# Optimization experiments

Hardware: AMD Instinct MI355X
Metric: run time of the kernel (lower is better)

Reference implementation:

```python
import jax, jax.numpy as jnp
import numpy as np

B, T_ENC, IN, H, TGT = 128, 128, 3, 512, 32

def setup_inputs() -> dict:
    key = jax.random.key(0)
    ks = jax.random.split(key, 16)
    s = 0.05
    return {
        "x": jax.random.normal(ks[0], (B, T_ENC, IN), jnp.float32),
        "y": jax.random.normal(ks[1], (B, TGT, 1), jnp.float32),
        # encoder: 2 layers x 2 directions (dim0 = [fwd, bwd])
        "enc_Wih0": jax.random.normal(ks[2], (2, H, IN), jnp.float32) * s,
        "enc_Whh0": jax.random.normal(ks[3], (2, H, H), jnp.float32) * s,
        "enc_Wih1": jax.random.normal(ks[4], (2, H, 2 * H), jnp.float32) * s,
        "enc_Whh1": jax.random.normal(ks[5], (2, H, H), jnp.float32) * s,
        "enc_bih": jax.random.normal(ks[6], (2, 2, H), jnp.float32) * s,  # (layer, dir, H)
        "enc_bhh": jax.random.normal(ks[7], (2, 2, H), jnp.float32) * s,
        # decoder: 4-layer unidirectional stack (matches hn shape (4,B,H))
        "dec_Wih0": jax.random.normal(ks[8], (H, IN), jnp.float32) * s,
        "dec_Wihr": jax.random.normal(ks[9], (3, H, H), jnp.float32) * s,
        "dec_Whh": jax.random.normal(ks[10], (4, H, H), jnp.float32) * s,
        "dec_bih": jax.random.normal(ks[11], (4, H), jnp.float32) * s,
        "dec_bhh": jax.random.normal(ks[12], (4, H), jnp.float32) * s,
        "lin_W": jax.random.normal(ks[13], (1, H), jnp.float32) * s,
        "lin_b": jax.random.normal(ks[14], (1,), jnp.float32) * s,
        "target_len": TGT,
        "teacher_forcing_ratio": 0,
    }

def _rnn_dir(x, Wih, Whh, bih, bhh, reverse):
    # x: (B,T,I) -> outputs (B,T,H), final carry (B,H)
    xs = jnp.einsum('bti,hi->tbh', x, Wih) + bih  # precompute input projection
    def step(h, xt):
        h = jnp.tanh(xt + h @ Whh.T + bhh)
        return h, h
    h0 = jnp.zeros((x.shape[0], Whh.shape[0]), x.dtype)
    hT, ys = jax.lax.scan(step, h0, xs, reverse=reverse)
    return jnp.transpose(ys, (1, 0, 2)), hT

def _forward(x, y, enc_Wih0, enc_Whh0, enc_Wih1, enc_Whh1, enc_bih, enc_bhh,
             dec_Wih0, dec_Wihr, dec_Whh, dec_bih, dec_bhh, lin_W, lin_b,
             target_len, teacher_forcing_ratio):
    # ---- bidirectional encoder, 2 layers ----
    of0, hf0 = _rnn_dir(x, enc_Wih0[0], enc_Whh0[0], enc_bih[0, 0], enc_bhh[0, 0], False)
    ob0, hb0 = _rnn_dir(x, enc_Wih0[1], enc_Whh0[1], enc_bih[0, 1], enc_bhh[0, 1], True)
    l0 = jnp.concatenate([of0, ob0], axis=-1)  # (B,T,2H)
    of1, hf1 = _rnn_dir(l0, enc_Wih1[0], enc_Whh1[0], enc_bih[1, 0], enc_bhh[1, 0], False)
    ob1, hb1 = _rnn_dir(l0, enc_Wih1[1], enc_Whh1[1], enc_bih[1, 1], enc_bhh[1, 1], True)
    hn = jnp.stack([hf0, hb0, hf1, hb1])  # (4,B,H), torch layer/dir ordering

    dec_in0 = x[:, -1, :]  # (B,IN)

    def dec_step(carry, _):
        hs, xin = carry
        inp = xin
        new_hs = []
        for l in range(4):
            Wih = dec_Wih0 if l == 0 else dec_Wihr[l - 1]
            h = jnp.tanh(inp @ Wih.T + dec_bih[l] + hs[l] @ dec_Whh[l].T + dec_bhh[l])
            new_hs.append(h)
            inp = h
        out = inp @ lin_W.T + lin_b  # (B,1)
        o0 = out[:, 0]
        s1 = xin[:, 0] - o0
        s2 = xin[:, 1] - s1
        nxt = jnp.stack([o0, s1, s2], axis=1)  # (B,3)
        return (jnp.stack(new_hs), nxt), out

    _, outs = jax.lax.scan(dec_step, (hn, dec_in0), None, length=target_len)
    return jnp.transpose(outs, (1, 0, 2))  # (B, target_len, 1)

def reference(x, y, enc_Wih0, enc_Whh0, enc_Wih1, enc_Whh1, enc_bih, enc_bhh,
              dec_Wih0, dec_Wihr, dec_Whh, dec_bih, dec_bhh, lin_W, lin_b,
              target_len, teacher_forcing_ratio):
    return _forward(x, y, enc_Wih0, enc_Whh0, enc_Wih1, enc_Whh1, enc_bih, enc_bhh,
                    dec_Wih0, dec_Wihr, dec_Whh, dec_bih, dec_bhh, lin_W, lin_b,
                    target_len, teacher_forcing_ratio)
```

## Files before the change

### kernel.cpp

```cpp
#include <hip/hip_runtime.h>
#include <cmath>

#define B 128
#define T 128
#define H 512
#define TGT 32

#define SCOPE_AGENT __HIP_MEMORY_SCOPE_AGENT

struct Args {
  const float *x, *eWih0, *eWhh0, *eWih1, *eWhh1, *ebih, *ebhh;
  const float *dWih0, *dWihr, *dWhh, *dbih, *dbhh, *linW, *linb;
  float *dst;
  float *xing;
  float *l0;
  unsigned *ctr;
  float *out;
};

__global__ void kinit(float* __restrict__ st, unsigned* __restrict__ ctr) {
  int idx = blockIdx.x * 256 + threadIdx.x;
  for (int i = idx; i < 4 * B * H; i += 256 * 256) st[i] = 0.f;
  if (idx < 64) ctr[idx] = 0u;
}

__device__ __forceinline__ void bumpR(unsigned* c) {
  __syncthreads();
  if (threadIdx.x == 0)
    __hip_atomic_fetch_add(c, 1u, __ATOMIC_RELAXED, SCOPE_AGENT);
}
__device__ __forceinline__ void waitcR(unsigned* c, unsigned tgt) {
  if (threadIdx.x == 0)
    while (__hip_atomic_load(c, __ATOMIC_RELAXED, SCOPE_AGENT) < tgt)
      __builtin_amdgcn_s_sleep(2);
  __syncthreads();
}
__device__ __forceinline__ void bumpF(unsigned* c) {
  __syncthreads();
  if (threadIdx.x == 0)
    __hip_atomic_fetch_add(c, 1u, __ATOMIC_RELEASE, SCOPE_AGENT);
}
__device__ __forceinline__ void waitcF(unsigned* c, unsigned tgt) {
  if (threadIdx.x == 0) {
    while (__hip_atomic_load(c, __ATOMIC_RELAXED, SCOPE_AGENT) < tgt)
      __builtin_amdgcn_s_sleep(2);
    __builtin_amdgcn_fence(__ATOMIC_ACQUIRE, "agent");
  }
  __syncthreads();
}

__device__ __forceinline__ void stC(float* p, float v) {
  __hip_atomic_store(p, v, __ATOMIC_RELAXED, SCOPE_AGENT);
}
__device__ __forceinline__ float ldC(const float* p) {
  return __hip_atomic_load(p, __ATOMIC_RELAXED, SCOPE_AGENT);
}

template <int ROWLEN, int GSTRIDE>
__device__ __forceinline__ void stage(const float* __restrict__ g,
                                      float* __restrict__ l, int rows, int lstride) {
  int total = rows * ROWLEN;
  for (int idx = (int)threadIdx.x * 4; idx < total; idx += 1024) {
    int r = idx / ROWLEN, k = idx - r * ROWLEN;
    float4 v = *(const float4*)(g + (size_t)r * GSTRIDE + k);
    *(float4*)(l + r * lstride + k) = v;
  }
}

__device__ __forceinline__ void stage16(const float* __restrict__ g,
                                        float* __restrict__ l) {
  const int t = threadIdx.x;
  const int r0 = t >> 7, k0 = (t & 127) * 4;
  float4 v[8];
#pragma unroll
  for (int i = 0; i < 8; i++)
    v[i] = *(const float4*)(g + (size_t)(r0 + 2 * i) * 512 + k0);
#pragma unroll
  for (int i = 0; i < 8; i++)
    *(float4*)(l + (r0 + 2 * i) * 516 + k0) = v[i];
}

__device__ __forceinline__ void stageC16(const float* __restrict__ g,
                                         float* __restrict__ l) {
  const unsigned long long* gu = (const unsigned long long*)g;
  unsigned long long* lu = (unsigned long long*)l;
  const int t = threadIdx.x;
  unsigned long long v[16];
#pragma unroll
  for (int i = 0; i < 16; i++)
    v[i] = __hip_atomic_load(gu + (size_t)i * 256 + t, __ATOMIC_RELAXED, SCOPE_AGENT);
#pragma unroll
  for (int i = 0; i < 16; i++)
    lu[i * 258 + t] = v[i];
}

#define DOT4(accv, hv, wv) accv += hv.x*wv.x + hv.y*wv.y + hv.z*wv.z + hv.w*wv.w
#define DOT4B(accv, hv, wv, iv, uv)                                       \
  accv += hv.x*wv.x + hv.y*wv.y + hv.z*wv.z + hv.w*wv.w                   \
        + iv.x*uv.x + iv.y*uv.y + iv.z*uv.z + iv.w*uv.w

__global__ __launch_bounds__(256, 1) void birnn_all(Args a) {
  __shared__ __align__(16) float sm[33088];
  const int tid = threadIdx.x;
  const int bx = blockIdx.x;

  {
    const int grp = bx & 15, mem = bx >> 4;
    const int dir = grp >> 3, btile = grp & 7, ntile = mem;
    const int b0 = btile * 16, n0 = ntile * 32;
    const int kg = tid & 7;
    const int ni = (tid >> 3) & 7;
    const int bi = tid >> 6;
    float* wl = sm;
    float* hl = sm + 16512;
    unsigned* c = a.ctr + dir * 8 + btile;

    stage<512, 512>(a.eWhh0 + (size_t)(dir * H + n0) * H, wl, 32, 516);

    const int nlane = n0 + ni * 4 + (kg & 3);
    const int r1 = bi * 4 + (kg >> 2);
    const int r2 = r1 + 2;
    float wx0 = a.eWih0[(dir * H + nlane) * 3 + 0];
    float wx1 = a.eWih0[(dir * H + nlane) * 3 + 1];
    float wx2 = a.eWih0[(dir * H + nlane) * 3 + 2];
    float bias = a.ebih[dir * H + nlane] + a.ebhh[dir * H + nlane];

    const float* hp0 = hl + (bi * 4 + 0) * 516 + kg * 4;
    const float* hp1 = hp0 + 516;
    const float* hp2 = hp0 + 2 * 516;
    const float* hp3 = hp0 + 3 * 516;
    const float* wp0 = wl + (ni * 4 + 0) * 516 + kg * 4;
    const float* wp1 = wp0 + 516;
    const float* wp2 = wp0 + 2 * 516;
    const float* wp3 = wp0 + 3 * 516;

    for (int s = 0; s < T; s++) {
      int t = dir ? (T - 1 - s) : s;
      const float* xr1 = a.x + ((size_t)(b0 + r1) * T + t) * 3;
      const float* xr2 = a.x + ((size_t)(b0 + r2) * T + t) * 3;
      float a1 = bias + xr1[0] * wx0 + xr1[1] * wx1 + xr1[2] * wx2;
      float a2 = bias + xr2[0] * wx0 + xr2[1] * wx1 + xr2[2] * wx2;

      if (s) waitcR(c, 16u * s); else __syncthreads();
      stageC16(a.dst + ((size_t)((s & 1) * 4 + dir) * B + b0) * H, hl);
      __syncthreads();

      float acc[4][4];
#pragma unroll
      for (int rr = 0; rr < 4; rr++)
#pragma unroll
        for (int cc = 0; cc < 4; cc++) acc[rr][cc] = 0.f;

#pragma unroll 4
      for (int i = 0; i < 16; i++) {
        const int k = i * 32;
        float4 h0 = *(const float4*)(hp0 + k);
        float4 h1 = *(const float4*)(hp1 + k);
        float4 h2 = *(const float4*)(hp2 + k);
        float4 h3 = *(const float4*)(hp3 + k);
        float4 w0 = *(const float4*)(wp0 + k);
        float4 w1 = *(const float4*)(wp1 + k);
        float4 w2 = *(const float4*)(wp2 + k);
        float4 w3 = *(const float4*)(wp3 + k);
        DOT4(acc[0][0], h0, w0); DOT4(acc[0][1], h0, w1); DOT4(acc[0][2], h0, w2); DOT4(acc[0][3], h0, w3);
        DOT4(acc[1][0], h1, w0); DOT4(acc[1][1], h1, w1); DOT4(acc[1][2], h1, w2); DOT4(acc[1][3], h1, w3);
        DOT4(acc[2][0], h2, w0); DOT4(acc[2][1], h2, w1); DOT4(acc[2][2], h2, w2); DOT4(acc[2][3], h2, w3);
        DOT4(acc[3][0], h3, w0); DOT4(acc[3][1], h3, w1); DOT4(acc[3][2], h3, w2); DOT4(acc[3][3], h3, w3);
      }
#pragma unroll
      for (int rr = 0; rr < 4; rr++)
#pragma unroll
        for (int cc = 0; cc < 4; cc++) {
          float v = acc[rr][cc];
          v += __shfl_xor(v, 1); v += __shfl_xor(v, 2); v += __shfl_xor(v, 4);
          acc[rr][cc] = v;
        }
      float s0v = 0.f, s1v = 0.f;
#pragma unroll
      for (int rr = 0; rr < 2; rr++)
#pragma unroll
        for (int cc = 0; cc < 4; cc++) {
          s0v = (kg == rr * 4 + cc) ? acc[rr][cc] : s0v;
          s1v = (kg == rr * 4 + cc) ? acc[rr + 2][cc] : s1v;
        }
      float o1 = tanhf(a1 + s0v);
      float o2 = tanhf(a2 + s1v);
      float* hw = a.dst + (size_t)(((s + 1) & 1) * 4 + dir) * B * H;
      stC(hw + (size_t)(b0 + r1) * H + nlane, o1);
      stC(hw + (size_t)(b0 + r2) * H + nlane, o2);
      bumpR(c);
      a.l0[((size_t)t * B + (b0 + r1)) * 1024 + dir * H + nlane] = o1;
      a.l0[((size_t)t * B + (b0 + r2)) * 1024 + dir * H + nlane] = o2;
    }
  }
  { unsigned* g = a.ctr + 40; bumpF(g); waitcF(g, 256u); }

  {
    float* xl = sm;
    float* wl = sm + 16448;
    const int kg = tid & 3;
    const int ci = (tid >> 2) & 15;
    const int ri = tid >> 6;
    for (int rt = 0; rt < 4; rt++) {
      int row0 = (bx * 4 + rt) * 16;
      __syncthreads();
      stage<1024, 1024>(a.l0 + (size_t)row0 * 1024, xl, 16, 1028);
      __syncthreads();
      for (int nc = 0; nc < 16; nc++) {
        const int nb = nc * 64 + ci * 4 + kg;
        float biasv = a.ebih[(2 + (nb >> 9)) * H + (nb & 511)] +
                      a.ebhh[(2 + (nb >> 9)) * H + (nb & 511)];
        float acc[4][4];
#pragma unroll
        for (int rr = 0; rr < 4; rr++)
#pragma unroll
          for (int cc = 0; cc < 4; cc++) acc[rr][cc] = 0.f;

        for (int kp = 0; kp < 4; kp++) {
          __syncthreads();
          stage<256, 1024>(a.eWih1 + (size_t)(nc * 64) * 1024 + kp * 256, wl, 64, 260);
          __syncthreads();
          const float* xp0 = xl + (ri * 4 + 0) * 1028 + kp * 256 + kg * 4;
          const float* xp1 = xp0 + 1028;
          const float* xp2 = xp0 + 2 * 1028;
          const float* xp3 = xp0 + 3 * 1028;
          const float* wq0 = wl + (ci * 4 + 0) * 260 + kg * 4;
          const float* wq1 = wq0 + 260;
          const float* wq2 = wq0 + 2 * 260;
// ... 9 lines not shown
            float4 w1 = *(const float4*)(wq1 + k);
            float4 w2 = *(const float4*)(wq2 + k);
            float4 w3 = *(const float4*)(wq3 + k);
            DOT4(acc[0][0], x0, w0); DOT4(acc[0][1], x0, w1); DOT4(acc[0][2], x0, w2); DOT4(acc[0][3], x0, w3);
            DOT4(acc[1][0], x1, w0); DOT4(acc[1][1], x1, w1); DOT4(acc[1][2], x1, w2); DOT4(acc[1][3], x1, w3);
            DOT4(acc[2][0], x2, w0); DOT4(acc[2][1], x2, w1); DOT4(acc[2][2], x2, w2); DOT4(acc[2][3], x2, w3);
            DOT4(acc[3][0], x3, w0); DOT4(acc[3][1], x3, w1); DOT4(acc[3][2], x3, w2); DOT4(acc[3][3], x3, w3);
          }
        }
#pragma unroll
        for (int rr = 0; rr < 4; rr++)
#pragma unroll
          for (int cc = 0; cc < 4; cc++) {
            float v = acc[rr][cc];
            v += __shfl_xor(v, 1); v += __shfl_xor(v, 2);
            acc[rr][cc] = v;
          }
        float o0 = 0.f, o1 = 0.f, o2 = 0.f, o3 = 0.f;
#pragma unroll
        for (int cc = 0; cc < 4; cc++) {
          o0 = (kg == cc) ? acc[0][cc] : o0;
          o1 = (kg == cc) ? acc[1][cc] : o1;
          o2 = (kg == cc) ? acc[2][cc] : o2;
          o3 = (kg == cc) ? acc[3][cc] : o3;
        }
        float* gr = a.l0 + (size_t)(row0 + ri * 4) * 1024 + nb;
        gr[0]        = o0 + biasv;
        gr[1024]     = o1 + biasv;
        gr[2 * 1024] = o2 + biasv;
        gr[3 * 1024] = o3 + biasv;
      }
    }
  }
  { unsigned* g = a.ctr + 40; bumpF(g); waitcF(g, 512u); }

  {
    const int grp = bx & 15, mem = bx >> 4;
    const int dir = grp >> 3, btile = grp & 7, ntile = mem;
    const int b0 = btile * 16, n0 = ntile * 32;
    const int kg = tid & 7;
    const int ni = (tid >> 3) & 7;
    const int bi = tid >> 6;
    float* wl = sm;
    float* hl = sm + 16512;
    unsigned* c = a.ctr + 16 + dir * 8 + btile;

    stage<512, 512>(a.eWhh1 + (size_t)(dir * H + n0) * H, wl, 32, 516);

    const int nlane = n0 + ni * 4 + (kg & 3);
    const int r1 = bi * 4 + (kg >> 2);
    const int r2 = r1 + 2;

    const float* hp0 = hl + (bi * 4 + 0) * 516 + kg * 4;
    const float* hp1 = hp0 + 516;
    const float* hp2 = hp0 + 2 * 516;
    const float* hp3 = hp0 + 3 * 516;
    const float* wp0 = wl + (ni * 4 + 0) * 516 + kg * 4;
    const float* wp1 = wp0 + 516;
    const float* wp2 = wp0 + 2 * 516;
    const float* wp3 = wp0 + 3 * 516;

    for (int s = 0; s < T; s++) {
      int t = dir ? (T - 1 - s) : s;
      float a1 = a.l0[((size_t)t * B + (b0 + r1)) * 1024 + dir * H + nlane];
      float a2 = a.l0[((size_t)t * B + (b0 + r2)) * 1024 + dir * H + nlane];

      if (s) waitcR(c, 16u * s); else __syncthreads();
      stageC16(a.dst + ((size_t)((s & 1) * 4 + 2 + dir) * B + b0) * H, hl);
      __syncthreads();

      float acc[4][4];
#pragma unroll
      for (int rr = 0; rr < 4; rr++)
#pragma unroll
        for (int cc = 0; cc < 4; cc++) acc[rr][cc] = 0.f;

#pragma unroll 4
      for (int i = 0; i < 16; i++) {
        const int k = i * 32;
        float4 h0 = *(const float4*)(hp0 + k);
        float4 h1 = *(const float4*)(hp1 + k);
        float4 h2 = *(const float4*)(hp2 + k);
        float4 h3 = *(const float4*)(hp3 + k);
        float4 w0 = *(const float4*)(wp0 + k);
        float4 w1 = *(const float4*)(wp1 + k);
        float4 w2 = *(const float4*)(wp2 + k);
        float4 w3 = *(const float4*)(wp3 + k);
        DOT4(acc[0][0], h0, w0); DOT4(acc[0][1], h0, w1); DOT4(acc[0][2], h0, w2); DOT4(acc[0][3], h0, w3);
        DOT4(acc[1][0], h1, w0); DOT4(acc[1][1], h1, w1); DOT4(acc[1][2], h1, w2); DOT4(acc[1][3], h1, w3);
        DOT4(acc[2][0], h2, w0); DOT4(acc[2][1], h2, w1); DOT4(acc[2][2], h2, w2); DOT4(acc[2][3], h2, w3);
        DOT4(acc[3][0], h3, w0); DOT4(acc[3][1], h3, w1); DOT4(acc[3][2], h3, w2); DOT4(acc[3][3], h3, w3);
      }
#pragma unroll
      for (int rr = 0; rr < 4; rr++)
#pragma unroll
        for (int cc = 0; cc < 4; cc++) {
          float v = acc[rr][cc];
          v += __shfl_xor(v, 1); v += __shfl_xor(v, 2); v += __shfl_xor(v, 4);
          acc[rr][cc] = v;
        }
      float s0v = 0.f, s1v = 0.f;
#pragma unroll
      for (int rr = 0; rr < 2; rr++)
#pragma unroll
        for (int cc = 0; cc < 4; cc++) {
          s0v = (kg == rr * 4 + cc) ? acc[rr][cc] : s0v;
          s1v = (kg == rr * 4 + cc) ? acc[rr + 2][cc] : s1v;
        }
      float o1 = tanhf(a1 + s0v);
      float o2 = tanhf(a2 + s1v);
      float* hw = a.dst + (size_t)(((s + 1) & 1) * 4 + 2 + dir) * B * H;
      stC(hw + (size_t)(b0 + r1) * H + nlane, o1);
      stC(hw + (size_t)(b0 + r2) * H + nlane, o2);
      bumpR(c);
    }
  }
  { unsigned* g = a.ctr + 40; bumpF(g); waitcF(g, 768u); }

  {
    const int btile = bx & 7, ntile = bx >> 3;
    const int b0 = btile * 16, n0 = ntile * 16;
    const int j = tid & 15, bl = tid >> 4;
    const int kg = tid & 15;
    const int ni = (tid >> 4) & 3;
    const int bi = tid >> 6;
    float* whh  = sm;
    float* wir  = sm + 8256;
    float* hlc  = sm + 16512;
    float* hin  = sm + 24768;
    float* xinL = sm + 33024;
    unsigned* c = a.ctr + 32 + btile;

    const int nlane = n0 + ni * 4 + (kg & 3);
    const int rloc  = bi * 4 + (kg >> 2);
    float w00 = a.dWih0[nlane * 3 + 0], w01 = a.dWih0[nlane * 3 + 1], w02 = a.dWih0[nlane * 3 + 2];
    float bias0 = a.dbih[0 * H + nlane] + a.dbhh[0 * H + nlane];
    float bias1 = a.dbih[1 * H + nlane] + a.dbhh[1 * H + nlane];
    float bias2 = a.dbih[2 * H + nlane] + a.dbhh[2 * H + nlane];
    float bias3 = a.dbih[3 * H + nlane] + a.dbhh[3 * H + nlane];

    const float* hp0 = hlc + (bi * 4 + 0) * 516 + kg * 4;
    const float* hp1 = hp0 + 516;
    const float* hp2 = hp0 + 2 * 516;
    const float* hp3 = hp0 + 3 * 516;
    const float* ip0 = hin + (bi * 4 + 0) * 516 + kg * 4;
    const float* ip1 = ip0 + 516;
    const float* ip2 = ip0 + 2 * 516;
    const float* ip3 = ip0 + 3 * 516;
    const float* wp0 = whh + (ni * 4 + 0) * 516 + kg * 4;
    const float* wp1 = wp0 + 516;
    const float* wp2 = wp0 + 2 * 516;
    const float* wp3 = wp0 + 3 * 516;
    const float* up0 = wir + (ni * 4 + 0) * 516 + kg * 4;
    const float* up1 = up0 + 516;
    const float* up2 = up0 + 2 * 516;
    const float* up3 = up0 + 3 * 516;

    stage16(a.dWhh + (size_t)(0 * H + n0) * H, whh);
    stageC16(a.dst + ((size_t)(0 * 4 + 0) * B + b0) * H, hlc);

    for (int m = 0; m < 128; m++) {
      int s = m >> 2, l = m & 3;
      int p = s & 1, q = 1 - p;
      if (m) waitcR(c, 32u * m); else __syncthreads();

      if (l) {
        stageC16(a.dst + ((size_t)(q * 4 + (l - 1)) * B + b0) * H, hin);
      } else if (s) {
        stageC16(a.dst + ((size_t)(p * 4 + 3) * B + b0) * H, hin);
      }
      __syncthreads();

      if (l == 0) {
        if (s == 0) {
          if (j == 0) {
            const float* xr = a.x + ((size_t)(b0 + bl) * T + (T - 1)) * 3;
            float v0 = xr[0], v1 = xr[1], v2 = xr[2];
            xinL[bl * 4 + 0] = v0; xinL[bl * 4 + 1] = v1; xinL[bl * 4 + 2] = v2;
            if (ntile == 0) {
              float* xw = a.xing + (size_t)(b0 + bl) * 4;
              stC(xw + 0, v0); stC(xw + 1, v1); stC(xw + 2, v2);
            }
          }
        } else {
          const float* h3r = hin + bl * 516;
          float v = 0.f;
          for (int k = j; k < H; k += 16) v += h3r[k] * a.linW[k];
          v += __shfl_xor(v, 8); v += __shfl_xor(v, 4);
          v += __shfl_xor(v, 2); v += __shfl_xor(v, 1);
          float o0 = v + a.linb[0];
          const float* xp = a.xing + ((size_t)((s - 1) & 1) * B + (b0 + bl)) * 4;
          float sv1 = ldC(xp + 0) - o0;
          float sv2 = ldC(xp + 1) - sv1;
          if (j == 0) {
            xinL[bl * 4 + 0] = o0; xinL[bl * 4 + 1] = sv1; xinL[bl * 4 + 2] = sv2;
            if (ntile == 0) {
              float* xw = a.xing + ((size_t)(s & 1) * B + (b0 + bl)) * 4;
// ... 50 lines not shown
          float4 h3 = *(const float4*)(hp3 + k);
          float4 w0 = *(const float4*)(wp0 + k);
          float4 w1 = *(const float4*)(wp1 + k);
          float4 w2 = *(const float4*)(wp2 + k);
          float4 w3 = *(const float4*)(wp3 + k);
          DOT4(acc[0][0], h0, w0); DOT4(acc[0][1], h0, w1); DOT4(acc[0][2], h0, w2); DOT4(acc[0][3], h0, w3);
          DOT4(acc[1][0], h1, w0); DOT4(acc[1][1], h1, w1); DOT4(acc[1][2], h1, w2); DOT4(acc[1][3], h1, w3);
          DOT4(acc[2][0], h2, w0); DOT4(acc[2][1], h2, w1); DOT4(acc[2][2], h2, w2); DOT4(acc[2][3], h2, w3);
          DOT4(acc[3][0], h3, w0); DOT4(acc[3][1], h3, w1); DOT4(acc[3][2], h3, w2); DOT4(acc[3][3], h3, w3);
        }
      }
#pragma unroll
      for (int rr = 0; rr < 4; rr++)
#pragma unroll
        for (int cc = 0; cc < 4; cc++) {
          float v = acc[rr][cc];
          v += __shfl_xor(v, 1); v += __shfl_xor(v, 2);
          v += __shfl_xor(v, 4); v += __shfl_xor(v, 8);
          acc[rr][cc] = v;
        }
      float sv = 0.f;
#pragma unroll
      for (int rr = 0; rr < 4; rr++)
#pragma unroll
        for (int cc = 0; cc < 4; cc++)
          sv = (kg == rr * 4 + cc) ? acc[rr][cc] : sv;

      float bs = (l == 0) ? bias0 : (l == 1) ? bias1 : (l == 2) ? bias2 : bias3;
      float at = bs;
      if (l == 0)
        at += xinL[rloc * 4 + 0] * w00 + xinL[rloc * 4 + 1] * w01 + xinL[rloc * 4 + 2] * w02;
      float hnew = tanhf(at + sv);
      stC(a.dst + ((size_t)(q * 4 + l) * B + (b0 + rloc)) * H + nlane, hnew);
      bumpR(c);

      if (m < 127) {
        int m2 = m + 1, l2 = m2 & 3, s2 = m2 >> 2, p2 = s2 & 1;
        stage16(a.dWhh + (size_t)(l2 * H + n0) * H, whh);
        if (l2)
          stage16(a.dWihr + (size_t)((l2 - 1) * H + n0) * H, wir);
        stageC16(a.dst + ((size_t)(p2 * 4 + l2) * B + b0) * H, hlc);
      }
    }

    if (ntile == 0) {
      waitcR(c, 32u * 128);
      const float* h3g = a.dst + ((size_t)(0 * 4 + 3) * B + (b0 + bl)) * H;
      float v = 0.f;
      for (int k = j; k < H; k += 16) v += ldC(h3g + k) * a.linW[k];
      v += __shfl_xor(v, 8); v += __shfl_xor(v, 4);
      v += __shfl_xor(v, 2); v += __shfl_xor(v, 1);
      if (j == 0) a.out[(size_t)(b0 + bl) * TGT + 31] = v + a.linb[0];
    }
  }
}

#undef DOT4
#undef DOT4B

extern "C" void kernel_launch(void* const* d_in, const int* in_sizes, int n_in,
                              void* d_out, int out_size, void* d_ws, size_t ws_size,
                              hipStream_t stream) {
  float* dst  = (float*)d_ws;
  float* xing = dst + 2 * 4 * B * H;
  unsigned* ctr = (unsigned*)((char*)d_ws + 2101248);
  float* l0 = (float*)((char*)d_ws + 2101504);

  kinit<<<256, 256, 0, stream>>>(dst, ctr);

  Args args;
  args.x     = (const float*)d_in[0];
  args.eWih0 = (const float*)d_in[2];
  args.eWhh0 = (const float*)d_in[3];
  args.eWih1 = (const float*)d_in[4];
  args.eWhh1 = (const float*)d_in[5];
  args.ebih  = (const float*)d_in[6];
  args.ebhh  = (const float*)d_in[7];
  args.dWih0 = (const float*)d_in[8];
  args.dWihr = (const float*)d_in[9];
// ... 12 lines not shown
```

Before: 4.724 ms.

## Interleave forward and backward encoder directions within each block

Each block now owns a 16-column tile of both the forward and backward recurrences of an encoder layer, and keeps both weight slices in shared memory. Within each time step it alternates fwd and bwd, so the wait on one direction's cross-block counter can overlap the other direction's matvec. The dot-product tiling changes to a 16-way K split with a shared dotK16 helper. The trade-off is that each step-barrier group now spans 32 blocks instead of 16, and the grid-wide counter moves to a new slot.

```diff
diff --git a/kernel.cpp b/kernel.cpp
--- a/kernel.cpp
+++ b/kernel.cpp
@@ -99,101 +99,103 @@
   accv += hv.x*wv.x + hv.y*wv.y + hv.z*wv.z + hv.w*wv.w                   \
         + iv.x*uv.x + iv.y*uv.y + iv.z*uv.z + iv.w*uv.w
 
+__device__ __forceinline__ float dotK16(const float* hb, const float* wb, int kg) {
+  float acc[4][4];
+#pragma unroll
+  for (int rr = 0; rr < 4; rr++)
+#pragma unroll
+    for (int cc = 0; cc < 4; cc++) acc[rr][cc] = 0.f;
+#pragma unroll
+  for (int i = 0; i < 8; i++) {
+    const int k = i * 64;
+    float4 h0 = *(const float4*)(hb + k);
+    float4 h1 = *(const float4*)(hb + 516 + k);
+    float4 h2 = *(const float4*)(hb + 1032 + k);
+    float4 h3 = *(const float4*)(hb + 1548 + k);
+    float4 w0 = *(const float4*)(wb + k);
+    float4 w1 = *(const float4*)(wb + 516 + k);
+    float4 w2 = *(const float4*)(wb + 1032 + k);
+    float4 w3 = *(const float4*)(wb + 1548 + k);
+    DOT4(acc[0][0],h0,w0); DOT4(acc[0][1],h0,w1); DOT4(acc[0][2],h0,w2); DOT4(acc[0][3],h0,w3);
+    DOT4(acc[1][0],h1,w0); DOT4(acc[1][1],h1,w1); DOT4(acc[1][2],h1,w2); DOT4(acc[1][3],h1,w3);
+    DOT4(acc[2][0],h2,w0); DOT4(acc[2][1],h2,w1); DOT4(acc[2][2],h2,w2); DOT4(acc[2][3],h2,w3);
+    DOT4(acc[3][0],h3,w0); DOT4(acc[3][1],h3,w1); DOT4(acc[3][2],h3,w2); DOT4(acc[3][3],h3,w3);
+  }
+#pragma unroll
+  for (int rr = 0; rr < 4; rr++)
+#pragma unroll
+    for (int cc = 0; cc < 4; cc++) {
+      float v = acc[rr][cc];
+      v += __shfl_xor(v, 1); v += __shfl_xor(v, 2);
+      v += __shfl_xor(v, 4); v += __shfl_xor(v, 8);
+      acc[rr][cc] = v;
+    }
+  float sv = 0.f;
+#pragma unroll
+  for (int rr = 0; rr < 4; rr++)
+#pragma unroll
+    for (int cc = 0; cc < 4; cc++)
+      sv = (kg == rr * 4 + cc) ? acc[rr][cc] : sv;
+  return sv;
+}
+
 __global__ __launch_bounds__(256, 1) void birnn_all(Args a) {
   __shared__ __align__(16) float sm[33088];
   const int tid = threadIdx.x;
   const int bx = blockIdx.x;
 
   {
-    const int grp = bx & 15, mem = bx >> 4;
-    const int dir = grp >> 3, btile = grp & 7, ntile = mem;
-    const int b0 = btile * 16, n0 = ntile * 32;
-    const int kg = tid & 7;
-    const int ni = (tid >> 3) & 7;
-    const int bi = tid >> 6;
-    float* wl = sm;
-    float* hl = sm + 16512;
-    unsigned* c = a.ctr + dir * 8 + btile;
-
-    stage<512, 512>(a.eWhh0 + (size_t)(dir * H + n0) * H, wl, 32, 516);
+    const int pt = bx & 7, ntile = bx >> 3;
+    const int b0 = pt * 16, n0 = ntile * 16;
+    const int kg = tid & 15, ni = (tid >> 4) & 3, bi = tid >> 6;
+    float* wl0 = sm;
+    float* wl1 = sm + 8256;
+    float* hl0 = sm + 16512;
+    float* hl1 = sm + 24768;
+    unsigned* cF = a.ctr + pt;
+    unsigned* cB = a.ctr + 8 + pt;
+
+    stage16(a.eWhh0 + (size_t)n0 * H, wl0);
+    stage16(a.eWhh0 + (size_t)(H + n0) * H, wl1);
 
     const int nlane = n0 + ni * 4 + (kg & 3);
-    const int r1 = bi * 4 + (kg >> 2);
-    const int r2 = r1 + 2;
-    float wx0 = a.eWih0[(dir * H + nlane) * 3 + 0];
-    float wx1 = a.eWih0[(dir * H + nlane) * 3 + 1];
-    float wx2 = a.eWih0[(dir * H + nlane) * 3 + 2];
-    float bias = a.ebih[dir * H + nlane] + a.ebhh[dir * H + nlane];
-
-    const float* hp0 = hl + (bi * 4 + 0) * 516 + kg * 4;
-    const float* hp1 = hp0 + 516;
-    const float* hp2 = hp0 + 2 * 516;
-    const float* hp3 = hp0 + 3 * 516;
-    const float* wp0 = wl + (ni * 4 + 0) * 516 + kg * 4;
-    const float* wp1 = wp0 + 516;
-    const float* wp2 = wp0 + 2 * 516;
-    const float* wp3 = wp0 + 3 * 516;
+    const int rloc  = bi * 4 + (kg >> 2);
+    float gwf0 = a.eWih0[(0 * H + nlane) * 3 + 0];
+    float gwf1 = a.eWih0[(0 * H + nlane) * 3 + 1];
+    float gwf2 = a.eWih0[(0 * H + nlane) * 3 + 2];
+    float gwb0 = a.eWih0[(1 * H + nlane) * 3 + 0];
+    float gwb1 = a.eWih0[(1 * H + nlane) * 3 + 1];
+    float gwb2 = a.eWih0[(1 * H + nlane) * 3 + 2];
+    float bf = a.ebih[nlane] + a.ebhh[nlane];
+    float bb = a.ebih[H + nlane] + a.ebhh[H + nlane];
+    const int hoff = bi * 4 * 516 + kg * 4;
+    const int woff = ni * 4 * 516 + kg * 4;
 
     for (int s = 0; s < T; s++) {
-      int t = dir ? (T - 1 - s) : s;
-      const float* xr1 = a.x + ((size_t)(b0 + r1) * T + t) * 3;
-      const float* xr2 = a.x + ((size_t)(b0 + r2) * T + t) * 3;
-      float a1 = bias + xr1[0] * wx0 + xr1[1] * wx1 + xr1[2] * wx2;
-      float a2 = bias + xr2[0] * wx0 + xr2[1] * wx1 + xr2[2] * wx2;
-
-      if (s) waitcR(c, 16u * s); else __syncthreads();
-      stageC16(a.dst + ((size_t)((s & 1) * 4 + dir) * B + b0) * H, hl);
-      __syncthreads();
-
-      float acc[4][4];
-#pragma unroll
-      for (int rr = 0; rr < 4; rr++)
-#pragma unroll
-        for (int cc = 0; cc < 4; cc++) acc[rr][cc] = 0.f;
-
-#pragma unroll 4
-      for (int i = 0; i < 16; i++) {
-        const int k = i * 32;
-        float4 h0 = *(const float4*)(hp0 + k);
-        float4 h1 = *(const float4*)(hp1 + k);
-        float4 h2 = *(const float4*)(hp2 + k);
-        float4 h3 = *(const float4*)(hp3 + k);
-        float4 w0 = *(const float4*)(wp0 + k);
-        float4 w1 = *(const float4*)(wp1 + k);
-        float4 w2 = *(const float4*)(wp2 + k);
-        float4 w3 = *(const float4*)(wp3 + k);
-        DOT4(acc[0][0], h0, w0); DOT4(acc[0][1], h0, w1); DOT4(acc[0][2], h0, w2); DOT4(acc[0][3], h0, w3);
-        DOT4(acc[1][0], h1, w0); DOT4(acc[1][1], h1, w1); DOT4(acc[1][2], h1, w2); DOT4(acc[1][3], h1, w3);
-        DOT4(acc[2][0], h2, w0); DOT4(acc[2][1], h2, w1); DOT4(acc[2][2], h2, w2); DOT4(acc[2][3], h2, w3);
-        DOT4(acc[3][0], h3, w0); DOT4(acc[3][1], h3, w1); DOT4(acc[3][2], h3, w2); DOT4(acc[3][3], h3, w3);
-      }
-#pragma unroll
-      for (int rr = 0; rr < 4; rr++)
-#pragma unroll
-        for (int cc = 0; cc < 4; cc++) {
-          float v = acc[rr][cc];
-          v += __shfl_xor(v, 1); v += __shfl_xor(v, 2); v += __shfl_xor(v, 4);
-          acc[rr][cc] = v;
-        }
-      float s0v = 0.f, s1v = 0.f;
-#pragma unroll
-      for (int rr = 0; rr < 2; rr++)
-#pragma unroll
-        for (int cc = 0; cc < 4; cc++) {
-          s0v = (kg == rr * 4 + cc) ? acc[rr][cc] : s0v;
-          s1v = (kg == rr * 4 + cc) ? acc[rr + 2][cc] : s1v;
-        }
-      float o1 = tanhf(a1 + s0v);
-      float o2 = tanhf(a2 + s1v);
-      float* hw = a.dst + (size_t)(((s + 1) & 1) * 4 + dir) * B * H;
-      stC(hw + (size_t)(b0 + r1) * H + nlane, o1);
-      stC(hw + (size_t)(b0 + r2) * H + nlane, o2);
-      bumpR(c);
-      a.l0[((size_t)t * B + (b0 + r1)) * 1024 + dir * H + nlane] = o1;
-      a.l0[((size_t)t * B + (b0 + r2)) * 1024 + dir * H + nlane] = o2;
+      int tf = s, tb = T - 1 - s;
+      const float* xrf = a.x + ((size_t)(b0 + rloc) * T + tf) * 3;
+      const float* xrb = a.x + ((size_t)(b0 + rloc) * T + tb) * 3;
+      float af = bf + xrf[0] * gwf0 + xrf[1] * gwf1 + xrf[2] * gwf2;
+      float ab = bb + xrb[0] * gwb0 + xrb[1] * gwb1 + xrb[2] * gwb2;
+
+      if (s) waitcR(cF, 32u * s); else __syncthreads();
+      stageC16(a.dst + ((size_t)((s & 1) * 4 + 0) * B + b0) * H, hl0);
+      __syncthreads();
+      float of = tanhf(af + dotK16(hl0 + hoff, wl0 + woff, kg));
+      stC(a.dst + ((size_t)(((s + 1) & 1) * 4 + 0) * B + (b0 + rloc)) * H + nlane, of);
+      bumpR(cF);
+      a.l0[((size_t)tf * B + (b0 + rloc)) * 1024 + nlane] = of;
+
+      if (s) waitcR(cB, 32u * s);
+      stageC16(a.dst + ((size_t)((s & 1) * 4 + 1) * B + b0) * H, hl1);
+      __syncthreads();
+      float ob = tanhf(ab + dotK16(hl1 + hoff, wl1 + woff, kg));
+      stC(a.dst + ((size_t)(((s + 1) & 1) * 4 + 1) * B + (b0 + rloc)) * H + nlane, ob);
+      bumpR(cB);
+      a.l0[((size_t)tb * B + (b0 + rloc)) * 1024 + H + nlane] = ob;
     }
   }
-  { unsigned* g = a.ctr + 40; bumpF(g); waitcF(g, 256u); }
+  { unsigned* g = a.ctr + 48; bumpF(g); waitcF(g, 256u); }
 
   {
     float* xl = sm;
@@ -269,90 +271,48 @@
       }
     }
   }
-  { unsigned* g = a.ctr + 40; bumpF(g); waitcF(g, 512u); }
+  { unsigned* g = a.ctr + 48; bumpF(g); waitcF(g, 512u); }
 
   {
-    const int grp = bx & 15, mem = bx >> 4;
-    const int dir = grp >> 3, btile = grp & 7, ntile = mem;
-    const int b0 = btile * 16, n0 = ntile * 32;
-    const int kg = tid & 7;
-    const int ni = (tid >> 3) & 7;
-    const int bi = tid >> 6;
-    float* wl = sm;
-    float* hl = sm + 16512;
-    unsigned* c = a.ctr + 16 + dir * 8 + btile;
-
-    stage<512, 512>(a.eWhh1 + (size_t)(dir * H + n0) * H, wl, 32, 516);
+    const int pt = bx & 7, ntile = bx >> 3;
+    const int b0 = pt * 16, n0 = ntile * 16;
+    const int kg = tid & 15, ni = (tid >> 4) & 3, bi = tid >> 6;
+    float* wl0 = sm;
+    float* wl1 = sm + 8256;
+    float* hl0 = sm + 16512;
+    float* hl1 = sm + 24768;
+    unsigned* cF = a.ctr + 16 + pt;
+    unsigned* cB = a.ctr + 24 + pt;
+
+    stage16(a.eWhh1 + (size_t)n0 * H, wl0);
+    stage16(a.eWhh1 + (size_t)(H + n0) * H, wl1);
 
     const int nlane = n0 + ni * 4 + (kg & 3);
-    const int r1 = bi * 4 + (kg >> 2);
-    const int r2 = r1 + 2;
-
-    const float* hp0 = hl + (bi * 4 + 0) * 516 + kg * 4;
-    const float* hp1 = hp0 + 516;
-    const float* hp2 = hp0 + 2 * 516;
-    const float* hp3 = hp0 + 3 * 516;
-    const float* wp0 = wl + (ni * 4 + 0) * 516 + kg * 4;
-    const float* wp1 = wp0 + 516;
-    const float* wp2 = wp0 + 2 * 516;
-    const float* wp3 = wp0 + 3 * 516;
+    const int rloc  = bi * 4 + (kg >> 2);
+    const int hoff = bi * 4 * 516 + kg * 4;
+    const int woff = ni * 4 * 516 + kg * 4;
 
     for (int s = 0; s < T; s++) {
-      int t = dir ? (T - 1 - s) : s;
-      float a1 = a.l0[((size_t)t * B + (b0 + r1)) * 1024 + dir * H + nlane];
-      float a2 = a.l0[((size_t)t * B + (b0 + r2)) * 1024 + dir * H + nlane];
-
-      if (s) waitcR(c, 16u * s); else __syncthreads();
-      stageC16(a.dst + ((size_t)((s & 1) * 4 + 2 + dir) * B + b0) * H, hl);
-      __syncthreads();
-
-      float acc[4][4];
-#pragma unroll
-      for (int rr = 0; rr < 4; rr++)
-#pragma unroll
-        for (int cc = 0; cc < 4; cc++) acc[rr][cc] = 0.f;
-
-#pragma unroll 4
-      for (int i = 0; i < 16; i++) {
-        const int k = i * 32;
-        float4 h0 = *(const float4*)(hp0 + k);
-        float4 h1 = *(const float4*)(hp1 + k);
-        float4 h2 = *(const float4*)(hp2 + k);
-        float4 h3 = *(const float4*)(hp3 + k);
-        float4 w0 = *(const float4*)(wp0 + k);
-        float4 w1 = *(const float4*)(wp1 + k);
-        float4 w2 = *(const float4*)(wp2 + k);
-        float4 w3 = *(const float4*)(wp3 + k);
-        DOT4(acc[0][0], h0, w0); DOT4(acc[0][1], h0, w1); DOT4(acc[0][2], h0, w2); DOT4(acc[0][3], h0, w3);
-        DOT4(acc[1][0], h1, w0); DOT4(acc[1][1], h1, w1); DOT4(acc[1][2], h1, w2); DOT4(acc[1][3], h1, w3);
-        DOT4(acc[2][0], h2, w0); DOT4(acc[2][1], h2, w1); DOT4(acc[2][2], h2, w2); DOT4(acc[2][3], h2, w3);
-        DOT4(acc[3][0], h3, w0); DOT4(acc[3][1], h3, w1); DOT4(acc[3][2], h3, w2); DOT4(acc[3][3], h3, w3);
-      }
-#pragma unroll
-      for (int rr = 0; rr < 4; rr++)
-#pragma unroll
-        for (int cc = 0; cc < 4; cc++) {
-          float v = acc[rr][cc];
-          v += __shfl_xor(v, 1); v += __shfl_xor(v, 2); v += __shfl_xor(v, 4);
-          acc[rr][cc] = v;
-        }
-      float s0v = 0.f, s1v = 0.f;
-#pragma unroll
-      for (int rr = 0; rr < 2; rr++)
-#pragma unroll
-        for (int cc = 0; cc < 4; cc++) {
-          s0v = (kg == rr * 4 + cc) ? acc[rr][cc] : s0v;
-          s1v = (kg == rr * 4 + cc) ? acc[rr + 2][cc] : s1v;
-        }
-      float o1 = tanhf(a1 + s0v);
-      float o2 = tanhf(a2 + s1v);
-      float* hw = a.dst + (size_t)(((s + 1) & 1) * 4 + 2 + dir) * B * H;
-      stC(hw + (size_t)(b0 + r1) * H + nlane, o1);
-      stC(hw + (size_t)(b0 + r2) * H + nlane, o2);
-      bumpR(c);
+      int tf = s, tb = T - 1 - s;
+      float af = a.l0[((size_t)tf * B + (b0 + rloc)) * 1024 + nlane];
+      float ab = a.l0[((size_t)tb * B + (b0 + rloc)) * 1024 + H + nlane];
+
+      if (s) waitcR(cF, 32u * s); else __syncthreads();
+      stageC16(a.dst + ((size_t)((s & 1) * 4 + 2) * B + b0) * H, hl0);
+      __syncthreads();
+      float of = tanhf(af + dotK16(hl0 + hoff, wl0 + woff, kg));
+      stC(a.dst + ((size_t)(((s + 1) & 1) * 4 + 2) * B + (b0 + rloc)) * H + nlane, of);
+      bumpR(cF);
+
+      if (s) waitcR(cB, 32u * s);
+      stageC16(a.dst + ((size_t)((s & 1) * 4 + 3) * B + b0) * H, hl1);
+      __syncthreads();
+      float ob = tanhf(ab + dotK16(hl1 + hoff, wl1 + woff, kg));
+      stC(a.dst + ((size_t)(((s + 1) & 1) * 4 + 3) * B + (b0 + rloc)) * H + nlane, ob);
+      bumpR(cB);
     }
   }
-  { unsigned* g = a.ctr + 40; bumpF(g); waitcF(g, 768u); }
+  { unsigned* g = a.ctr + 48; bumpF(g); waitcF(g, 768u); }
 
   {
     const int btile = bx & 7, ntile = bx >> 3;
```

New measurement: 5.706 ms. +20.8%, slower.

## Retile encoder recurrence to 8-row batch tiles with 64-column weight slices

Applied to the files above, without the earlier changes.

Changes the encoder recurrent layers' work split from 16 batch rows x 32 hidden columns per block to 8 batch rows x 64 columns, giving 16 batch tiles per direction, each synchronised by its own counter over 8 member blocks. Each step now stages a smaller hidden-state slab (8 rows) from global memory, and each sync group has fewer members, which is meant to cut per-step barrier latency and staging traffic. In exchange each block holds twice as many weight rows in shared memory, the LDS footprint grows, and counter indices move, with layer-1 waits offset by the layer-0 count. Inner-loop arithmetic per thread is unchanged.

```diff
diff --git a/kernel.cpp b/kernel.cpp
--- a/kernel.cpp
+++ b/kernel.cpp
@@ -94,55 +94,72 @@
     lu[i * 258 + t] = v[i];
 }
 
+__device__ __forceinline__ void stageC8(const float* __restrict__ g,
+                                        float* __restrict__ l) {
+  const unsigned long long* gu = (const unsigned long long*)g;
+  unsigned long long* lu = (unsigned long long*)l;
+  const int t = threadIdx.x;
+  unsigned long long v[8];
+#pragma unroll
+  for (int i = 0; i < 8; i++)
+    v[i] = __hip_atomic_load(gu + (size_t)i * 256 + t, __ATOMIC_RELAXED, SCOPE_AGENT);
+#pragma unroll
+  for (int i = 0; i < 8; i++)
+    lu[i * 258 + t] = v[i];
+}
+
 #define DOT4(accv, hv, wv) accv += hv.x*wv.x + hv.y*wv.y + hv.z*wv.z + hv.w*wv.w
 #define DOT4B(accv, hv, wv, iv, uv)                                       \
   accv += hv.x*wv.x + hv.y*wv.y + hv.z*wv.z + hv.w*wv.w                   \
         + iv.x*uv.x + iv.y*uv.y + iv.z*uv.z + iv.w*uv.w
 
 __global__ __launch_bounds__(256, 1) void birnn_all(Args a) {
-  __shared__ __align__(16) float sm[33088];
+  __shared__ __align__(16) float sm[37152];
   const int tid = threadIdx.x;
   const int bx = blockIdx.x;
 
+  const int dirE = bx >> 7, btE = (bx >> 3) & 15, ntE = bx & 7;
+  const int b0E = btE * 8, n0E = ntE * 64;
+  const int kgE = tid & 7, niE = (tid >> 3) & 15, biE = tid >> 7;
+  const int nlaneE = n0E + niE * 4 + (kgE & 3);
+  const int r1E = biE * 4 + (kgE >> 2);
+  const int r2E = r1E + 2;
+  const int hoffE = biE * 4 * 516 + kgE * 4;
+  const int woffE = niE * 4 * 516 + kgE * 4;
+
   {
-    const int grp = bx & 15, mem = bx >> 4;
-    const int dir = grp >> 3, btile = grp & 7, ntile = mem;
-    const int b0 = btile * 16, n0 = ntile * 32;
-    const int kg = tid & 7;
-    const int ni = (tid >> 3) & 7;
-    const int bi = tid >> 6;
     float* wl = sm;
-    float* hl = sm + 16512;
-    unsigned* c = a.ctr + dir * 8 + btile;
-
-    stage<512, 512>(a.eWhh0 + (size_t)(dir * H + n0) * H, wl, 32, 516);
-
-    const int nlane = n0 + ni * 4 + (kg & 3);
-    const int r1 = bi * 4 + (kg >> 2);
-    const int r2 = r1 + 2;
-    float wx0 = a.eWih0[(dir * H + nlane) * 3 + 0];
-    float wx1 = a.eWih0[(dir * H + nlane) * 3 + 1];
-    float wx2 = a.eWih0[(dir * H + nlane) * 3 + 2];
-    float bias = a.ebih[dir * H + nlane] + a.ebhh[dir * H + nlane];
-
-    const float* hp0 = hl + (bi * 4 + 0) * 516 + kg * 4;
+    float* hl = sm + 33024;
+    unsigned* c = a.ctr + dirE * 16 + btE;
+
+    stage16(a.eWhh0 + (size_t)(dirE * H + n0E) * H, wl);
+    stage16(a.eWhh0 + (size_t)(dirE * H + n0E + 16) * H, wl + 16 * 516);
+    stage16(a.eWhh0 + (size_t)(dirE * H + n0E + 32) * H, wl + 32 * 516);
+    stage16(a.eWhh0 + (size_t)(dirE * H + n0E + 48) * H, wl + 48 * 516);
+
+    float wx0 = a.eWih0[(dirE * H + nlaneE) * 3 + 0];
+    float wx1 = a.eWih0[(dirE * H + nlaneE) * 3 + 1];
+    float wx2 = a.eWih0[(dirE * H + nlaneE) * 3 + 2];
+    float bias = a.ebih[dirE * H + nlaneE] + a.ebhh[dirE * H + nlaneE];
+
+    const float* hp0 = hl + hoffE;
     const float* hp1 = hp0 + 516;
     const float* hp2 = hp0 + 2 * 516;
     const float* hp3 = hp0 + 3 * 516;
-    const float* wp0 = wl + (ni * 4 + 0) * 516 + kg * 4;
+    const float* wp0 = wl + woffE;
     const float* wp1 = wp0 + 516;
     const float* wp2 = wp0 + 2 * 516;
     const float* wp3 = wp0 + 3 * 516;
 
     for (int s = 0; s < T; s++) {
-      int t = dir ? (T - 1 - s) : s;
-      const float* xr1 = a.x + ((size_t)(b0 + r1) * T + t) * 3;
-      const float* xr2 = a.x + ((size_t)(b0 + r2) * T + t) * 3;
+      int t_ = dirE ? (T - 1 - s) : s;
+      const float* xr1 = a.x + ((size_t)(b0E + r1E) * T + t_) * 3;
+      const float* xr2 = a.x + ((size_t)(b0E + r2E) * T + t_) * 3;
       float a1 = bias + xr1[0] * wx0 + xr1[1] * wx1 + xr1[2] * wx2;
       float a2 = bias + xr2[0] * wx0 + xr2[1] * wx1 + xr2[2] * wx2;
 
-      if (s) waitcR(c, 16u * s); else __syncthreads();
-      stageC16(a.dst + ((size_t)((s & 1) * 4 + dir) * B + b0) * H, hl);
+      if (s) waitcR(c, 8u * s); else __syncthreads();
+      stageC8(a.dst + ((size_t)((s & 1) * 4 + dirE) * B + b0E) * H, hl);
       __syncthreads();
 
       float acc[4][4];
@@ -162,10 +179,10 @@
         float4 w1 = *(const float4*)(wp1 + k);
         float4 w2 = *(const float4*)(wp2 + k);
         float4 w3 = *(const float4*)(wp3 + k);
-        DOT4(acc[0][0], h0, w0); DOT4(acc[0][1], h0, w1); DOT4(acc[0][2], h0, w2); DOT4(acc[0][3], h0, w3);
-        DOT4(acc[1][0], h1, w0); DOT4(acc[1][1], h1, w1); DOT4(acc[1][2], h1, w2); DOT4(acc[1][3], h1, w3);
-        DOT4(acc[2][0], h2, w0); DOT4(acc[2][1], h2, w1); DOT4(acc[2][2], h2, w2); DOT4(acc[2][3], h2, w3);
-        DOT4(acc[3][0], h3, w0); DOT4(acc[3][1], h3, w1); DOT4(acc[3][2], h3, w2); DOT4(acc[3][3], h3, w3);
+        DOT4(acc[0][0],h0,w0); DOT4(acc[0][1],h0,w1); DOT4(acc[0][2],h0,w2); DOT4(acc[0][3],h0,w3);
+        DOT4(acc[1][0],h1,w0); DOT4(acc[1][1],h1,w1); DOT4(acc[1][2],h1,w2); DOT4(acc[1][3],h1,w3);
+        DOT4(acc[2][0],h2,w0); DOT4(acc[2][1],h2,w1); DOT4(acc[2][2],h2,w2); DOT4(acc[2][3],h2,w3);
+        DOT4(acc[3][0],h3,w0); DOT4(acc[3][1],h3,w1); DOT4(acc[3][2],h3,w2); DOT4(acc[3][3],h3,w3);
       }
 #pragma unroll
       for (int rr = 0; rr < 4; rr++)
@@ -180,20 +197,20 @@
       for (int rr = 0; rr < 2; rr++)
 #pragma unroll
         for (int cc = 0; cc < 4; cc++) {
-          s0v = (kg == rr * 4 + cc) ? acc[rr][cc] : s0v;
-          s1v = (kg == rr * 4 + cc) ? acc[rr + 2][cc] : s1v;
+          s0v = (kgE == rr * 4 + cc) ? acc[rr][cc] : s0v;
+          s1v = (kgE == rr * 4 + cc) ? acc[rr + 2][cc] : s1v;
         }
       float o1 = tanhf(a1 + s0v);
       float o2 = tanhf(a2 + s1v);
-      float* hw = a.dst + (size_t)(((s + 1) & 1) * 4 + dir) * B * H;
-      stC(hw + (size_t)(b0 + r1) * H + nlane, o1);
-      stC(hw + (size_t)(b0 + r2) * H + nlane, o2);
+      float* hw = a.dst + (size_t)(((s + 1) & 1) * 4 + dirE) * B * H;
+      stC(hw + (size_t)(b0E + r1E) * H + nlaneE, o1);
+      stC(hw + (size_t)(b0E + r2E) * H + nlaneE, o2);
       bumpR(c);
-      a.l0[((size_t)t * B + (b0 + r1)) * 1024 + dir * H + nlane] = o1;
-      a.l0[((size_t)t * B + (b0 + r2)) * 1024 + dir * H + nlane] = o2;
+      a.l0[((size_t)t_ * B + (b0E + r1E)) * 1024 + dirE * H + nlaneE] = o1;
+      a.l0[((size_t)t_ * B + (b0E + r2E)) * 1024 + dirE * H + nlaneE] = o2;
     }
   }
-  { unsigned* g = a.ctr + 40; bumpF(g); waitcF(g, 256u); }
+  { unsigned* g = a.ctr + 48; bumpF(g); waitcF(g, 256u); }
 
   {
     float* xl = sm;
@@ -269,41 +286,35 @@
       }
     }
   }
-  { unsigned* g = a.ctr + 40; bumpF(g); waitcF(g, 512u); }
+  { unsigned* g = a.ctr + 48; bumpF(g); waitcF(g, 512u); }
 
   {
-    const int grp = bx & 15, mem = bx >> 4;
-    const int dir = grp >> 3, btile = grp & 7, ntile = mem;
-    const int b0 = btile * 16, n0 = ntile * 32;
-    const int kg = tid & 7;
-    const int ni = (tid >> 3) & 7;
-    const int bi = tid >> 6;
     float* wl = sm;
-    float* hl = sm + 16512;
-    unsigned* c = a.ctr + 16 + dir * 8 + btile;
-
-    stage<512, 512>(a.eWhh1 + (size_t)(dir * H + n0) * H, wl, 32, 516);
-
-    const int nlane = n0 + ni * 4 + (kg & 3);
-    const int r1 = bi * 4 + (kg >> 2);
-    const int r2 = r1 + 2;
-
-    const float* hp0 = hl + (bi * 4 + 0) * 516 + kg * 4;
+    float* hl = sm + 33024;
+    unsigned* c = a.ctr + dirE * 16 + btE;
+    const unsigned base = 8u * T;
+
+    stage16(a.eWhh1 + (size_t)(dirE * H + n0E) * H, wl);
+    stage16(a.eWhh1 + (size_t)(dirE * H + n0E + 16) * H, wl + 16 * 516);
+    stage16(a.eWhh1 + (size_t)(dirE * H + n0E + 32) * H, wl + 32 * 516);
+    stage16(a.eWhh1 + (size_t)(dirE * H + n0E + 48) * H, wl + 48 * 516);
+
+    const float* hp0 = hl + hoffE;
     const float* hp1 = hp0 + 516;
     const float* hp2 = hp0 + 2 * 516;
     const float* hp3 = hp0 + 3 * 516;
-    const float* wp0 = wl + (ni * 4 + 0) * 516 + kg * 4;
+    const float* wp0 = wl + woffE;
     const float* wp1 = wp0 + 516;
     const float* wp2 = wp0 + 2 * 516;
     const float* wp3 = wp0 + 3 * 516;
 
     for (int s = 0; s < T; s++) {
-      int t = dir ? (T - 1 - s) : s;
-      float a1 = a.l0[((size_t)t * B + (b0 + r1)) * 1024 + dir * H + nlane];
-      float a2 = a.l0[((size_t)t * B + (b0 + r2)) * 1024 + dir * H + nlane];
-
-      if (s) waitcR(c, 16u * s); else __syncthreads();
-      stageC16(a.dst + ((size_t)((s & 1) * 4 + 2 + dir) * B + b0) * H, hl);
+      int t_ = dirE ? (T - 1 - s) : s;
+      float a1 = a.l0[((size_t)t_ * B + (b0E + r1E)) * 1024 + dirE * H + nlaneE];
+      float a2 = a.l0[((size_t)t_ * B + (b0E + r2E)) * 1024 + dirE * H + nlaneE];
+
+      if (s) waitcR(c, base + 8u * s); else __syncthreads();
+      stageC8(a.dst + ((size_t)((s & 1) * 4 + 2 + dirE) * B + b0E) * H, hl);
       __syncthreads();
 
       float acc[4][4];
@@ -323,10 +334,10 @@
         float4 w1 = *(const float4*)(wp1 + k);
         float4 w2 = *(const float4*)(wp2 + k);
         float4 w3 = *(const float4*)(wp3 + k);
-        DOT4(acc[0][0], h0, w0); DOT4(acc[0][1], h0, w1); DOT4(acc[0][2], h0, w2); DOT4(acc[0][3], h0, w3);
-        DOT4(acc[1][0], h1, w0); DOT4(acc[1][1], h1, w1); DOT4(acc[1][2], h1, w2); DOT4(acc[1][3], h1, w3);
-        DOT4(acc[2][0], h2, w0); DOT4(acc[2][1], h2, w1); DOT4(acc[2][2], h2, w2); DOT4(acc[2][3], h2, w3);
-        DOT4(acc[3][0], h3, w0); DOT4(acc[3][1], h3, w1); DOT4(acc[3][2], h3, w2); DOT4(acc[3][3], h3, w3);
+        DOT4(acc[0][0],h0,w0); DOT4(acc[0][1],h0,w1); DOT4(acc[0][2],h0,w2); DOT4(acc[0][3],h0,w3);
+        DOT4(acc[1][0],h1,w0); DOT4(acc[1][1],h1,w1); DOT4(acc[1][2],h1,w2); DOT4(acc[1][3],h1,w3);
+        DOT4(acc[2][0],h2,w0); DOT4(acc[2][1],h2,w1); DOT4(acc[2][2],h2,w2); DOT4(acc[2][3],h2,w3);
+        DOT4(acc[3][0],h3,w0); DOT4(acc[3][1],h3,w1); DOT4(acc[3][2],h3,w2); DOT4(acc[3][3],h3,w3);
       }
 #pragma unroll
       for (int rr = 0; rr < 4; rr++)
@@ -341,18 +352,18 @@
       for (int rr = 0; rr < 2; rr++)
 #pragma unroll
         for (int cc = 0; cc < 4; cc++) {
-          s0v = (kg == rr * 4 + cc) ? acc[rr][cc] : s0v;
-          s1v = (kg == rr * 4 + cc) ? acc[rr + 2][cc] : s1v;
+          s0v = (kgE == rr * 4 + cc) ? acc[rr][cc] : s0v;
+          s1v = (kgE == rr * 4 + cc) ? acc[rr + 2][cc] : s1v;
         }
       float o1 = tanhf(a1 + s0v);
       float o2 = tanhf(a2 + s1v);
-      float* hw = a.dst + (size_t)(((s + 1) & 1) * 4 + 2 + dir) * B * H;
-      stC(hw + (size_t)(b0 + r1) * H + nlane, o1);
-      stC(hw + (size_t)(b0 + r2) * H + nlane, o2);
+      float* hw = a.dst + (size_t)(((s + 1) & 1) * 4 + 2 + dirE) * B * H;
+      stC(hw + (size_t)(b0E + r1E) * H + nlaneE, o1);
+      stC(hw + (size_t)(b0E + r2E) * H + nlaneE, o2);
       bumpR(c);
     }
   }
-  { unsigned* g = a.ctr + 40; bumpF(g); waitcF(g, 768u); }
+  { unsigned* g = a.ctr + 48; bumpF(g); waitcF(g, 768u); }
 
   {
     const int btile = bx & 7, ntile = bx >> 3;
```

After: 5.624 ms. 1.19x slower.

## Replace shared atomic step counters with per-block flag slots polled by min

Applied to the files above, without the earlier changes.

Each block in a group now writes its own progress value into a separate flag slot with a plain relaxed store, and waiters poll all slots in the group and take the minimum. This replaces a single counter that every block hit with an atomic add, with the aim of removing serialization on one contended address. The flag slots reuse the workspace region after xing, at word 3 of each 16-byte record, and kinit now zeroes them. Weight staging also switches to two stage16 calls. The trade-off is that the polling thread issues 16 or 32 loads per spin instead of one.

```diff
diff --git a/kernel.cpp b/kernel.cpp
--- a/kernel.cpp
+++ b/kernel.cpp
@@ -22,17 +22,29 @@
   int idx = blockIdx.x * 256 + threadIdx.x;
   for (int i = idx; i < 4 * B * H; i += 256 * 256) st[i] = 0.f;
   if (idx < 64) ctr[idx] = 0u;
-}
-
-__device__ __forceinline__ void bumpR(unsigned* c) {
+  if (idx < 256) ((unsigned*)(st + (size_t)2 * 4 * B * H))[idx * 4 + 3] = 0u;
+}
+
+__device__ __forceinline__ void relF(unsigned* U, int slot, unsigned val) {
   __syncthreads();
   if (threadIdx.x == 0)
-    __hip_atomic_fetch_add(c, 1u, __ATOMIC_RELAXED, SCOPE_AGENT);
-}
-__device__ __forceinline__ void waitcR(unsigned* c, unsigned tgt) {
-  if (threadIdx.x == 0)
-    while (__hip_atomic_load(c, __ATOMIC_RELAXED, SCOPE_AGENT) < tgt)
+    __hip_atomic_store(U + 4 * slot + 3, val, __ATOMIC_RELAXED, SCOPE_AGENT);
+}
+template <int NP>
+__device__ __forceinline__ void waitF(unsigned* U, int slot0, unsigned tgt) {
+  if (threadIdx.x == 0) {
+    for (;;) {
+      unsigned mn = 0xffffffffu;
+#pragma unroll
+      for (int p = 0; p < NP; p++) {
+        unsigned v = __hip_atomic_load(U + 4 * (slot0 + p) + 3,
+                                       __ATOMIC_RELAXED, SCOPE_AGENT);
+        mn = v < mn ? v : mn;
+      }
+      if (mn >= tgt) break;
       __builtin_amdgcn_s_sleep(2);
+    }
+  }
   __syncthreads();
 }
 __device__ __forceinline__ void bumpF(unsigned* c) {
@@ -103,6 +115,7 @@
   __shared__ __align__(16) float sm[33088];
   const int tid = threadIdx.x;
   const int bx = blockIdx.x;
+  unsigned* U = (unsigned*)a.xing;
 
   {
     const int grp = bx & 15, mem = bx >> 4;
@@ -113,9 +126,10 @@
     const int bi = tid >> 6;
     float* wl = sm;
     float* hl = sm + 16512;
-    unsigned* c = a.ctr + dir * 8 + btile;
-
-    stage<512, 512>(a.eWhh0 + (size_t)(dir * H + n0) * H, wl, 32, 516);
+    const int g16 = (dir * 8 + btile) * 16;
+
+    stage16(a.eWhh0 + (size_t)(dir * H + n0) * H, wl);
+    stage16(a.eWhh0 + (size_t)(dir * H + n0 + 16) * H, wl + 16 * 516);
 
     const int nlane = n0 + ni * 4 + (kg & 3);
     const int r1 = bi * 4 + (kg >> 2);
@@ -141,7 +155,7 @@
       float a1 = bias + xr1[0] * wx0 + xr1[1] * wx1 + xr1[2] * wx2;
       float a2 = bias + xr2[0] * wx0 + xr2[1] * wx1 + xr2[2] * wx2;
 
-      if (s) waitcR(c, 16u * s); else __syncthreads();
+      if (s) waitF<16>(U, g16, (unsigned)s); else __syncthreads();
       stageC16(a.dst + ((size_t)((s & 1) * 4 + dir) * B + b0) * H, hl);
       __syncthreads();
 
@@ -188,7 +202,7 @@
       float* hw = a.dst + (size_t)(((s + 1) & 1) * 4 + dir) * B * H;
       stC(hw + (size_t)(b0 + r1) * H + nlane, o1);
       stC(hw + (size_t)(b0 + r2) * H + nlane, o2);
-      bumpR(c);
+      relF(U, g16 + ntile, (unsigned)(s + 1));
       a.l0[((size_t)t * B + (b0 + r1)) * 1024 + dir * H + nlane] = o1;
       a.l0[((size_t)t * B + (b0 + r2)) * 1024 + dir * H + nlane] = o2;
     }
@@ -280,9 +294,10 @@
     const int bi = tid >> 6;
     float* wl = sm;
     float* hl = sm + 16512;
-    unsigned* c = a.ctr + 16 + dir * 8 + btile;
-
-    stage<512, 512>(a.eWhh1 + (size_t)(dir * H + n0) * H, wl, 32, 516);
+    const int g16 = (dir * 8 + btile) * 16;
+
+    stage16(a.eWhh1 + (size_t)(dir * H + n0) * H, wl);
+    stage16(a.eWhh1 + (size_t)(dir * H + n0 + 16) * H, wl + 16 * 516);
 
     const int nlane = n0 + ni * 4 + (kg & 3);
     const int r1 = bi * 4 + (kg >> 2);
@@ -302,7 +317,7 @@
       float a1 = a.l0[((size_t)t * B + (b0 + r1)) * 1024 + dir * H + nlane];
       float a2 = a.l0[((size_t)t * B + (b0 + r2)) * 1024 + dir * H + nlane];
 
-      if (s) waitcR(c, 16u * s); else __syncthreads();
+      if (s) waitF<16>(U, g16, (unsigned)(T + s)); else __syncthreads();
       stageC16(a.dst + ((size_t)((s & 1) * 4 + 2 + dir) * B + b0) * H, hl);
       __syncthreads();
 
@@ -349,7 +364,7 @@
       float* hw = a.dst + (size_t)(((s + 1) & 1) * 4 + 2 + dir) * B * H;
       stC(hw + (size_t)(b0 + r1) * H + nlane, o1);
       stC(hw + (size_t)(b0 + r2) * H + nlane, o2);
-      bumpR(c);
+      relF(U, g16 + ntile, (unsigned)(T + s + 1));
     }
   }
   { unsigned* g = a.ctr + 40; bumpF(g); waitcF(g, 768u); }
@@ -366,7 +381,7 @@
     float* hlc  = sm + 16512;
     float* hin  = sm + 24768;
     float* xinL = sm + 33024;
-    unsigned* c = a.ctr + 32 + btile;
+    const int g32 = btile * 32;
 
     const int nlane = n0 + ni * 4 + (kg & 3);
     const int rloc  = bi * 4 + (kg >> 2);
@@ -399,7 +414,7 @@
     for (int m = 0; m < 128; m++) {
       int s = m >> 2, l = m & 3;
       int p = s & 1, q = 1 - p;
-      if (m) waitcR(c, 32u * m); else __syncthreads();
+      if (m) waitF<32>(U, g32, (unsigned)(2 * T + m)); else __syncthreads();
 
       if (l) {
         stageC16(a.dst + ((size_t)(q * 4 + (l - 1)) * B + b0) * H, hin);
@@ -516,7 +531,7 @@
         at += xinL[rloc * 4 + 0] * w00 + xinL[rloc * 4 + 1] * w01 + xinL[rloc * 4 + 2] * w02;
       float hnew = tanhf(at + sv);
       stC(a.dst + ((size_t)(q * 4 + l) * B + (b0 + rloc)) * H + nlane, hnew);
-      bumpR(c);
+      relF(U, g32 + ntile, (unsigned)(2 * T + m + 1));
 
       if (m < 127) {
         int m2 = m + 1, l2 = m2 & 3, s2 = m2 >> 2, p2 = s2 & 1;
@@ -528,7 +543,7 @@
     }
 
     if (ntile == 0) {
-      waitcR(c, 32u * 128);
+      waitF<32>(U, g32, (unsigned)(2 * T + 128));
       const float* h3g = a.dst + ((size_t)(0 * 4 + 3) * B + (b0 + bl)) * H;
       float v = 0.f;
       for (int k = j; k < H; k += 16) v += ldC(h3g + k) * a.linW[k];
```

Result: no change. 4.674 ms (median of 2 runs) (-1.1%).
